# Kernel optimization log

Hardware: AMD Instinct MI355X
Metric: run time of the kernel (lower is better)

## Reference

```python
import jax, jax.numpy as jnp
import numpy as np

N_SH, N_U, N_I = 1195, 805, 390   # hard-coded in KDHR
D = 64                            # embedding_dim / latent_dim
B = 65536                         # prescription batch
E_SH = 100000
BN_EPS = 1e-5


def setup_inputs() -> dict:
    key = jax.random.key(0)
    ks = jax.random.split(key, 20)
    s = 0.02
    return {
        "edge_index_SH": jax.random.randint(ks[0], (2, E_SH), 0, N_SH),
        "edge_index_SS": jax.random.randint(ks[1], (2, 50000), 0, N_U),
        "edge_index_HH": jax.random.randint(ks[2], (2, 50000), 0, N_I),
        "prescription": jax.random.uniform(ks[3], (B, N_I), dtype=jnp.float32),
        "sh_emb": jax.random.normal(ks[4], (N_SH, D), dtype=jnp.float32) * s,
        # GCNConv_SH layer 1 and 2 (Linear weights, torch layout [out,in])
        "W1": jax.random.normal(ks[5], (D, D), dtype=jnp.float32) * s,
        "b1": jnp.zeros((D,), jnp.float32),
        "W2": jax.random.normal(ks[6], (D, D), dtype=jnp.float32) * s,
        "b2": jnp.zeros((D,), jnp.float32),
        # proj = Linear(64,64) -> ELU -> Linear(64,64)
        "Wp1": jax.random.normal(ks[7], (D, D), dtype=jnp.float32) * s,
        "bp1": jnp.zeros((D,), jnp.float32),
        "Wp2": jax.random.normal(ks[8], (D, D), dtype=jnp.float32) * s,
        "bp2": jnp.zeros((D,), jnp.float32),
        # self.mlp = Linear(64,64); self.SI_bn = BatchNorm1d(64)
        "Wm": jax.random.normal(ks[9], (D, D), dtype=jnp.float32) * s,
        "bm": jnp.zeros((D,), jnp.float32),
        "bn_gamma": jnp.ones((D,), jnp.float32),
        "bn_beta": jnp.zeros((D,), jnp.float32),
    }


def _gcn_layer(x, W, b, src, dst):
    # GCNConv_SH: message = lin(x_j), aggr='mean' at dst, then tanh
    m = x[src] @ W.T + b                                   # [E, D]
    s = jax.ops.segment_sum(m, dst, num_segments=N_SH)     # [N_SH, D]
    cnt = jax.ops.segment_sum(jnp.ones(dst.shape, x.dtype), dst, num_segments=N_SH)
    return jnp.tanh(s / jnp.maximum(cnt, 1.0)[:, None])


def _l2n(z):
    return z / jnp.linalg.norm(z, axis=1, keepdims=True)


def reference(edge_index_SH, edge_index_SS, edge_index_HH, prescription,
              sh_emb, W1, b1, W2, b2, Wp1, bp1, Wp2, bp2, Wm, bm,
              bn_gamma, bn_beta):
    src, dst = edge_index_SH[0], edge_index_SH[1]
    h1 = _gcn_layer(sh_emb, W1, b1, src, dst)
    h2 = _gcn_layer(h1, W2, b2, src, dst)                  # x_SH6
    c_emb_u, c_emb_i = h2[:N_U], h2[N_U:]                  # [805,64], [390,64]

    def proj(z):
        return jax.nn.elu(z @ Wp1.T + bp1) @ Wp2.T + bp2

    # Same2Loss projected+normalized embeddings (c_u: herbs 390, c_i: users 805)
    es = _l2n(proj(c_emb_i))                               # [390, 64]
    eh = _l2n(proj(c_emb_u))                               # [805, 64]

    e_synd = prescription @ es                             # [B, 64]
    pre_sum = jnp.sum(prescription, axis=1, keepdims=True)
    e = e_synd / pre_sum
    e = e @ Wm.T + bm                                      # mlp
    mu = jnp.mean(e, axis=0)                               # BatchNorm1d (train)
    var = jnp.var(e, axis=0)
    e = (e - mu) * jax.lax.rsqrt(var + BN_EPS) * bn_gamma + bn_beta
    e = jax.nn.relu(e)
    return e @ eh.T                                        # [B, 805]
```

## Files before the change

kernel.cpp:

```cpp
#include <hip/hip_runtime.h>
#include <math.h>

#define NSH 1195
#define NU  805
#define NI  390
#define DD  64
#define BROWS 65536
#define ESH 100000
#define KPAD 416
#define NUPAD 832

typedef _Float16 f16;
typedef _Float16 f16x2 __attribute__((ext_vector_type(2)));
typedef _Float16 f16x8 __attribute__((ext_vector_type(8)));
typedef float f32x4 __attribute__((ext_vector_type(4)));

#define OFF_STATS  0u
#define OFF_ESWT   128u
#define OFF_EH     13440u
#define OFF_ROWPTR 41344u
#define OFF_CURSOR 42624u
#define OFF_COLIDX 43904u
#define OFF_H1     144000u
#define OFF_EPRE   220480u

__global__ __launch_bounds__(1024) void prep_kernel(const int* __restrict__ edges,
                                                    int* __restrict__ row_ptr,
                                                    int* __restrict__ cursor,
                                                    float* __restrict__ stats,
                                                    f16* __restrict__ esWT) {
    __shared__ int s[2048];
    __shared__ int h[1280];
    int t = threadIdx.x;
    h[t] = 0;
    if (t + 1024 < 1280) h[t + 1024] = 0;
    if (t < 128) stats[t] = 0.f;
    if (t < 832) {
        int d = t / 13, j = t - d * 13;
        *(uint32_t*)&esWT[d * KPAD + 390 + j * 2] = 0u;
    }
    __syncthreads();
    for (int e = t; e < ESH; e += 1024)
        atomicAdd(&h[edges[ESH + e]], 1);
    __syncthreads();
    s[t] = (t < NSH) ? h[t] : 0;
    s[t + 1024] = (t + 1024 < NSH) ? h[t + 1024] : 0;
    __syncthreads();
    for (int off = 1; off < 2048; off <<= 1) {
        int a = s[t], b = s[t + 1024];
        int aa = (t >= off) ? s[t - off] : 0;
        int bb = s[t + 1024 - off];
        __syncthreads();
        s[t] = a + aa;
        s[t + 1024] = b + bb;
        __syncthreads();
    }
    if (t == 0) row_ptr[0] = 0;
    for (int i = t; i < NSH; i += 1024) {
        row_ptr[i + 1] = s[i];
        cursor[i] = (i == 0) ? 0 : s[i - 1];
    }
}

__global__ __launch_bounds__(256) void scatter_kernel(const int* __restrict__ edges,
                                                      int* __restrict__ cursor,
                                                      int* __restrict__ col_idx) {
    int e = blockIdx.x * 256 + threadIdx.x;
    if (e < ESH) {
        int t = edges[ESH + e];
        int pos = atomicAdd(&cursor[t], 1);
        col_idx[pos] = edges[e];
    }
}

__global__ __launch_bounds__(256) void gcn_gather1(const int* __restrict__ row_ptr,
                                                   const int* __restrict__ col_idx,
                                                   const float* __restrict__ x,
                                                   const float* __restrict__ W,
                                                   const float* __restrict__ b,
                                                   float* __restrict__ out) {
    __shared__ float s_wt[DD * DD];
    __shared__ float s_p[4 * DD];
    int tid = threadIdx.x;
    int w = tid >> 6, lane = tid & 63;
    for (int i = tid; i < DD * DD; i += 256) {
        int j = i >> 6, k = i & 63;
        s_wt[k * DD + j] = W[i];
    }
    int node = blockIdx.x;
    int beg = row_ptr[node], end = row_ptr[node + 1];
    float acc = 0.f;
    for (int e = beg + w; e < end; e += 4)
        acc += x[col_idx[e] * DD + lane];
    s_p[w * DD + lane] = acc;
    __syncthreads();
    float z = s_p[lane] + s_p[DD + lane] + s_p[2 * DD + lane] + s_p[3 * DD + lane];
    __syncthreads();
    if (w == 0) s_p[lane] = z;
    __syncthreads();
    float cntf = (float)(end - beg);
    float o = cntf * b[lane];
    #pragma unroll 8
    for (int k = 0; k < DD; k++)
        o = fmaf(s_p[k], s_wt[k * DD + lane], o);
    float h = tanhf(o / fmaxf(cntf, 1.f));
    if (w == 0) out[node * DD + lane] = h;
}

__global__ __launch_bounds__(256) void gcn2_fused(const int* __restrict__ row_ptr,
                                                  const int* __restrict__ col_idx,
                                                  const float* __restrict__ h1,
                                                  const float* __restrict__ W2,
                                                  const float* __restrict__ b2,
                                                  const float* __restrict__ Wp1,
                                                  const float* __restrict__ bp1,
                                                  const float* __restrict__ Wp2,
                                                  const float* __restrict__ bp2,
                                                  const float* __restrict__ Wm,
                                                  f16* __restrict__ eh16,
                                                  f16* __restrict__ esWT) {
    __shared__ float s_w2[DD * DD], s_p1[DD * DD], s_p2[DD * DD], s_wm[DD * DD];
    __shared__ float s_v[4 * DD];
    int tid = threadIdx.x;
    int w = tid >> 6, lane = tid & 63;
    for (int i = tid; i < DD * DD; i += 256) {
        int j = i >> 6, k = i & 63;
        s_w2[k * DD + j] = W2[i];
        s_p1[k * DD + j] = Wp1[i];
        s_p2[k * DD + j] = Wp2[i];
        s_wm[k * DD + j] = Wm[i];
    }
    int node = blockIdx.x;
    int beg = row_ptr[node], end = row_ptr[node + 1];
    float acc = 0.f;
    for (int e = beg + w; e < end; e += 4)
        acc += h1[col_idx[e] * DD + lane];
    s_v[w * DD + lane] = acc;
    __syncthreads();
    float z = s_v[lane] + s_v[DD + lane] + s_v[2 * DD + lane] + s_v[3 * DD + lane];
    __syncthreads();
    if (w == 0) s_v[lane] = z;
    __syncthreads();
    float cntf = (float)(end - beg);
    float o = cntf * b2[lane];
    #pragma unroll 8
    for (int k = 0; k < DD; k++)
        o = fmaf(s_v[k], s_w2[k * DD + lane], o);
    float h2v = tanhf(o / fmaxf(cntf, 1.f));
    __syncthreads();
    if (w == 0) s_v[lane] = h2v;
    __syncthreads();
    float t = bp1[lane];
    #pragma unroll 8
    for (int k = 0; k < DD; k++)
        t = fmaf(s_v[k], s_p1[k * DD + lane], t);
    t = t > 0.f ? t : expm1f(t);
    __syncthreads();
    if (w == 0) s_v[lane] = t;
    __syncthreads();
    float o2 = bp2[lane];
    #pragma unroll 8
    for (int k = 0; k < DD; k++)
        o2 = fmaf(s_v[k], s_p2[k * DD + lane], o2);
    float sq = o2 * o2;
    #pragma unroll
    for (int off = 1; off < 64; off <<= 1) sq += __shfl_xor(sq, off);
    float r = o2 / sqrtf(sq);
    if (node < NU) {
        if (w == 0) eh16[node * DD + lane] = (f16)r;
    } else {
        __syncthreads();
        if (w == 0) s_v[lane] = r;
        __syncthreads();
        float m = 0.f;
        #pragma unroll 8
        for (int k = 0; k < DD; k++)
            m = fmaf(s_v[k], s_wm[k * DD + lane], m);
        if (w == 0) esWT[lane * KPAD + (node - NU)] = (f16)m;
    }
}

__global__ __launch_bounds__(256) void synd_v2(const float* __restrict__ P,
                                               const f16* __restrict__ esWT,
                                               const float* __restrict__ bm,
                                               float* __restrict__ e_pre,
                                               float* __restrict__ stats) {
    __shared__ __align__(16) f16 s_P[64 * KPAD];
    __shared__ float s_stats[128];
    int tid = threadIdx.x;
    if (tid < 128) s_stats[tid] = 0.f;

    for (int i = tid; i < 64 * 13; i += 256) {
        int row = i / 13, j = i - row * 13;
        *(uint32_t*)&s_P[row * KPAD + 390 + j * 2] = 0u;
    }
    const float* Pb = P + (size_t)blockIdx.x * 64 * NI;
    for (int it = 0; it < 25; it++) {
        int f = it * 1024 + tid * 4;
        if (f < 64 * NI) {
            f32x4 v = *(const f32x4*)(Pb + f);
            int row = f / NI;
            int col = f - row * NI;
            *(f16x2*)&s_P[row * KPAD + col] = (f16x2){(f16)v.x, (f16)v.y};
            int row2 = row, col2 = col + 2;
            if (col2 == NI) { row2 = row + 1; col2 = 0; }
            *(f16x2*)&s_P[row2 * KPAD + col2] = (f16x2){(f16)v.z, (f16)v.w};
        }
    }
    __syncthreads();

    int lane = tid & 63, w = tid >> 6;
    int l15 = lane & 15, lk = lane >> 4;
    int rowbase = blockIdx.x * 64 + w * 16;

    f32x4 acc[5];
    #pragma unroll
    for (int ni = 0; ni < 5; ni++) acc[ni] = (f32x4){0.f, 0.f, 0.f, 0.f};

    f16x8 ones;
    #pragma unroll
    for (int i = 0; i < 8; i++) ones[i] = (f16)1.0f;

    const f16* arow = &s_P[(w * 16 + l15) * KPAD];
    const f16* bp[4];
    #pragma unroll
    for (int ni = 0; ni < 4; ni++)
        bp[ni] = esWT + (size_t)(ni * 16 + l15) * KPAD;

    for (int step = 0; step < 13; step++) {
        int kb = step * 32 + lk * 8;
        f16x8 a = *(const f16x8*)(arow + kb);
        f16x8 bfr[4];
        #pragma unroll
        for (int ni = 0; ni < 4; ni++)
            bfr[ni] = *(const f16x8*)(bp[ni] + kb);
        #pragma unroll
        for (int ni = 0; ni < 4; ni++)
            acc[ni] = __builtin_amdgcn_mfma_f32_16x16x32_f16(a, bfr[ni], acc[ni], 0, 0, 0);
        acc[4] = __builtin_amdgcn_mfma_f32_16x16x32_f16(a, ones, acc[4], 0, 0, 0);
    }

    float bmv[4];
    #pragma unroll
    for (int ni = 0; ni < 4; ni++) bmv[ni] = bm[ni * 16 + l15];

    #pragma unroll
    for (int ni = 0; ni < 4; ni++) {
        float s = 0.f, q = 0.f;
        #pragma unroll
        for (int j = 0; j < 4; j++) {
            float v = acc[ni][j] / acc[4][j] + bmv[ni];
            int row = rowbase + lk * 4 + j;
            e_pre[(size_t)row * DD + ni * 16 + l15] = v;
            s += v;
            q = fmaf(v, v, q);
        }
        s += __shfl_xor(s, 16); s += __shfl_xor(s, 32);
        q += __shfl_xor(q, 16); q += __shfl_xor(q, 32);
        if (lk == 0) {
            atomicAdd(&s_stats[ni * 16 + l15], s);
            atomicAdd(&s_stats[64 + ni * 16 + l15], q);
        }
    }
    __syncthreads();
    if (tid < 128) atomicAdd(&stats[tid], s_stats[tid]);
}

__global__ __launch_bounds__(256) void out_fused(const float* __restrict__ e_pre,
                                                 const f16* __restrict__ eh16,
                                                 const float* __restrict__ stats,
                                                 const float* __restrict__ gamma,
                                                 const float* __restrict__ beta,
                                                 float* __restrict__ out) {
    __shared__ __align__(16) f16 s_eh[256 * DD];
    __shared__ float s_bn[128];
    int tid = threadIdx.x;
    int cg = blockIdx.x;
    int t0 = (cg == 0) ? 0 : cg * 3 + 1;
    int nt = (cg == 0) ? 4 : 3;
    int cbase = t0 * 64;
    int nrows = nt * 64;

    if (tid < 64) {
        float mu  = stats[tid] * (1.0f / 65536.0f);
        float ex2 = stats[64 + tid] * (1.0f / 65536.0f);
        float var = ex2 - mu * mu;
        float rstd = 1.0f / sqrtf(var + 1e-5f);
        float sc = rstd * gamma[tid];
        s_bn[tid] = sc;
        s_bn[64 + tid] = beta[tid] - mu * sc;
    }

    const uint4* src = (const uint4*)(eh16 + (size_t)cbase * DD);
    int nchunks = nrows * 8;
    for (int c = tid; c < nchunks; c += 256) {
        int row = c >> 3, slot = c & 7;
        uint4 v = src[c];
        *(uint4*)&s_eh[row * DD + ((slot ^ (row & 7)) << 3)] = v;
    }
    __syncthreads();

    int lane = tid & 63, w = tid >> 6;
    int l15 = lane & 15, lk = lane >> 4;
    int r0 = blockIdx.y * 64 + w * 16;

    f16x8 afr[2];
    {
        const float* pr = e_pre + (size_t)(r0 + l15) * DD;
        #pragma unroll
        for (int ks = 0; ks < 2; ks++) {
            int kb = ks * 32 + lk * 8;
            f32x4 v0 = *(const f32x4*)&pr[kb];
            f32x4 v1 = *(const f32x4*)&pr[kb + 4];
            f16x8 a;
            #pragma unroll
            for (int i = 0; i < 4; i++) {
                a[i]     = (f16)fmaxf(fmaf(v0[i], s_bn[kb + i],     s_bn[64 + kb + i]),     0.f);
                a[4 + i] = (f16)fmaxf(fmaf(v1[i], s_bn[kb + 4 + i], s_bn[64 + kb + 4 + i]), 0.f);
            }
            afr[ks] = a;
        }
    }

    for (int tt = 0; tt < nt; tt++) {
        f32x4 acc[4];
        #pragma unroll
        for (int c16 = 0; c16 < 4; c16++) acc[c16] = (f32x4){0.f, 0.f, 0.f, 0.f};
        #pragma unroll
        for (int c16 = 0; c16 < 4; c16++) {
            int lc = tt * 64 + c16 * 16 + l15;
            #pragma unroll
            for (int ks = 0; ks < 2; ks++) {
                int slot = (ks * 4 + lk) ^ (lc & 7);
                f16x8 b = *(const f16x8*)&s_eh[lc * DD + (slot << 3)];
                acc[c16] = __builtin_amdgcn_mfma_f32_16x16x32_f16(afr[ks], b, acc[c16], 0, 0, 0);
            }
        }
        #pragma unroll
        for (int c16 = 0; c16 < 4; c16++) {
            int col = cbase + tt * 64 + c16 * 16 + l15;
            if (col < NU) {
                #pragma unroll
                for (int j = 0; j < 4; j++) {
                    int row = r0 + lk * 4 + j;
                    out[(size_t)row * NU + col] = acc[c16][j];
                }
            }
        }
    }
}

extern "C" void kernel_launch(void* const* d_in, const int* in_sizes, int n_in,
                              void* d_out, int out_size, void* d_ws, size_t ws_size,
                              hipStream_t stream) {
    const int*   eSH   = (const int*)d_in[0];
    const float* presc = (const float*)d_in[3];
    const float* shemb = (const float*)d_in[4];
    const float* W1  = (const float*)d_in[5];
    const float* b1  = (const float*)d_in[6];
    const float* W2  = (const float*)d_in[7];
    const float* b2  = (const float*)d_in[8];
    const float* Wp1 = (const float*)d_in[9];
    const float* bp1 = (const float*)d_in[10];
    const float* Wp2 = (const float*)d_in[11];
    const float* bp2 = (const float*)d_in[12];
    const float* Wm  = (const float*)d_in[13];
    const float* bm  = (const float*)d_in[14];
    const float* gam = (const float*)d_in[15];
    const float* bet = (const float*)d_in[16];

    float* ws    = (float*)d_ws;
    float* stats = ws + OFF_STATS;
    f16*   esWT  = (f16*)(ws + OFF_ESWT);
    f16*   eh16  = (f16*)(ws + OFF_EH);
    int*   rowp  = (int*)(ws + OFF_ROWPTR);
    int*   curs  = (int*)(ws + OFF_CURSOR);
    int*   cidx  = (int*)(ws + OFF_COLIDX);
    float* h1    = ws + OFF_H1;
    float* e_pre = ws + OFF_EPRE;
    float* out   = (float*)d_out;

    prep_kernel<<<1, 1024, 0, stream>>>(eSH, rowp, curs, stats, esWT);
    scatter_kernel<<<391, 256, 0, stream>>>(eSH, curs, cidx);
    gcn_gather1<<<NSH, 256, 0, stream>>>(rowp, cidx, shemb, W1, b1, h1);
    gcn2_fused<<<NSH, 256, 0, stream>>>(rowp, cidx, h1, W2, b2,
                                        Wp1, bp1, Wp2, bp2, Wm, eh16, esWT);
    synd_v2<<<1024, 256, 0, stream>>>(presc, esWT, bm, e_pre, stats);
    out_fused<<<dim3(4, 1024), 256, 0, stream>>>(e_pre, eh16, stats, gam, bet, out);
}
```

Measured before the change: 241.9 us.

## Replace CSR graph aggregation with dense adjacency matrix MFMA GEMMs

Drops the CSR build (single-block histogram/scan plus scatter) and per-node gather kernels. Instead it builds a dense fp32 count adjacency matrix with atomics and runs both GCN layers plus the projection MLPs as fp16 MFMA matrix multiplies over 64-node tiles. Degree counts come from an extra MFMA against a ones vector. This removes the serial prep kernel and irregular gathers, but adds zeroing and reading of a ~1216x1216 dense matrix, runs the graph stage on only 19 blocks, and lowers the graph stage to fp16 precision. The matrix reuses the e_pre workspace, which is safe only because it is consumed before synd_v2 writes e_pre.

```diff
diff --git a/kernel.cpp b/kernel.cpp
--- a/kernel.cpp
+++ b/kernel.cpp
@@ -9,6 +9,7 @@
 #define ESH 100000
 #define KPAD 416
 #define NUPAD 832
+#define KA  1216
 
 typedef _Float16 f16;
 typedef _Float16 f16x2 __attribute__((ext_vector_type(2)));
@@ -18,166 +19,240 @@
 #define OFF_STATS  0u
 #define OFF_ESWT   128u
 #define OFF_EH     13440u
-#define OFF_ROWPTR 41344u
-#define OFF_CURSOR 42624u
-#define OFF_COLIDX 43904u
-#define OFF_H1     144000u
-#define OFF_EPRE   220480u
-
-__global__ __launch_bounds__(1024) void prep_kernel(const int* __restrict__ edges,
-                                                    int* __restrict__ row_ptr,
-                                                    int* __restrict__ cursor,
-                                                    float* __restrict__ stats,
-                                                    f16* __restrict__ esWT) {
-    __shared__ int s[2048];
-    __shared__ int h[1280];
-    int t = threadIdx.x;
-    h[t] = 0;
-    if (t + 1024 < 1280) h[t + 1024] = 0;
-    if (t < 128) stats[t] = 0.f;
-    if (t < 832) {
-        int d = t / 13, j = t - d * 13;
-        *(uint32_t*)&esWT[d * KPAD + 390 + j * 2] = 0u;
-    }
+#define OFF_SHEMBT 40064u
+#define OFF_H1T    78976u
+#define OFF_EPRE   117888u
+
+__global__ __launch_bounds__(256) void prep_kernel(const float* __restrict__ shemb,
+                                                   float* __restrict__ A,
+                                                   f16* __restrict__ shembT,
+                                                   float* __restrict__ stats,
+                                                   f16* __restrict__ esWT,
+                                                   f16* __restrict__ eh16) {
+    int b = blockIdx.x, tid = threadIdx.x;
+    if (b < 1444) {
+        int i = b * 256 + tid;
+        *(f32x4*)&A[i * 4] = (f32x4){0.f, 0.f, 0.f, 0.f};
+    } else if (b < 1748) {
+        int i = (b - 1444) * 256 + tid;
+        int d = i / KA, k = i - d * KA;
+        shembT[i] = (k < NSH) ? (f16)shemb[k * DD + d] : (f16)0.f;
+    } else {
+        for (int i = tid; i < 128; i += 256) stats[i] = 0.f;
+        for (int i = tid; i < 832; i += 256) {
+            int d = i / 13, j = i - d * 13;
+            *(uint32_t*)&esWT[d * KPAD + 390 + j * 2] = 0u;
+        }
+        for (int i = tid; i < 864; i += 256)
+            ((uint32_t*)eh16)[NU * 32 + i] = 0u;
+    }
+}
+
+__global__ __launch_bounds__(256) void build_A(const int* __restrict__ edges,
+                                               float* __restrict__ A) {
+    int e = blockIdx.x * 256 + threadIdx.x;
+    if (e < ESH)
+        atomicAdd(&A[edges[ESH + e] * KA + edges[e]], 1.0f);
+}
+
+__global__ __launch_bounds__(256) void gcn1_mfma(const float* __restrict__ A,
+                                                 const f16* __restrict__ shembT,
+                                                 const float* __restrict__ W1,
+                                                 const float* __restrict__ b1,
+                                                 f16* __restrict__ h1T) {
+    __shared__ __align__(16) f16 s_w1[DD * 72];
+    __shared__ __align__(16) f16 s_agg[4][16 * 72];
+    int tid = threadIdx.x;
+    for (int i = tid; i < DD * DD; i += 256)
+        s_w1[(i >> 6) * 72 + (i & 63)] = (f16)W1[i];
     __syncthreads();
-    for (int e = t; e < ESH; e += 1024)
-        atomicAdd(&h[edges[ESH + e]], 1);
+
+    int lane = tid & 63, w = tid >> 6;
+    int l15 = lane & 15, lk = lane >> 4;
+    int mbase = blockIdx.x * 64 + w * 16;
+
+    f16x8 ones;
+    #pragma unroll
+    for (int i = 0; i < 8; i++) ones[i] = (f16)1.0f;
+
+    f32x4 acc[4], accC = (f32x4){0.f, 0.f, 0.f, 0.f};
+    #pragma unroll
+    for (int ni = 0; ni < 4; ni++) acc[ni] = (f32x4){0.f, 0.f, 0.f, 0.f};
+    const float* arow = A + (size_t)(mbase + l15) * KA;
+    for (int step = 0; step < 38; step++) {
+        int kb = step * 32 + lk * 8;
+        f32x4 q0 = *(const f32x4*)(arow + kb);
+        f32x4 q1 = *(const f32x4*)(arow + kb + 4);
+        f16x8 a;
+        a[0] = (f16)q0.x; a[1] = (f16)q0.y; a[2] = (f16)q0.z; a[3] = (f16)q0.w;
+        a[4] = (f16)q1.x; a[5] = (f16)q1.y; a[6] = (f16)q1.z; a[7] = (f16)q1.w;
+        #pragma unroll
+        for (int ni = 0; ni < 4; ni++) {
+            f16x8 bf = *(const f16x8*)&shembT[(ni * 16 + l15) * KA + kb];
+            acc[ni] = __builtin_amdgcn_mfma_f32_16x16x32_f16(a, bf, acc[ni], 0, 0, 0);
+        }
+        accC = __builtin_amdgcn_mfma_f32_16x16x32_f16(a, ones, accC, 0, 0, 0);
+    }
+    #pragma unroll
+    for (int ni = 0; ni < 4; ni++)
+        #pragma unroll
+        for (int j = 0; j < 4; j++)
+            s_agg[w][(lk * 4 + j) * 72 + ni * 16 + l15] = (f16)acc[ni][j];
+
+    f16x8 a2[2];
+    a2[0] = *(const f16x8*)&s_agg[w][l15 * 72 + lk * 8];
+    a2[1] = *(const f16x8*)&s_agg[w][l15 * 72 + 32 + lk * 8];
+    f32x4 p[4];
+    #pragma unroll
+    for (int ni = 0; ni < 4; ni++) p[ni] = (f32x4){0.f, 0.f, 0.f, 0.f};
+    #pragma unroll
+    for (int ks = 0; ks < 2; ks++)
+        #pragma unroll
+        for (int ni = 0; ni < 4; ni++) {
+            f16x8 bf = *(const f16x8*)&s_w1[(ni * 16 + l15) * 72 + ks * 32 + lk * 8];
+            p[ni] = __builtin_amdgcn_mfma_f32_16x16x32_f16(a2[ks], bf, p[ni], 0, 0, 0);
+        }
+    #pragma unroll
+    for (int ni = 0; ni < 4; ni++) {
+        int n = ni * 16 + l15;
+        float bn = b1[n];
+        #pragma unroll
+        for (int j = 0; j < 4; j++) {
+            float cnt = accC[j];
+            float h = tanhf(fmaf(cnt, bn, p[ni][j]) / fmaxf(cnt, 1.f));
+            h1T[n * KA + mbase + lk * 4 + j] = (f16)h;
+        }
+    }
+}
+
+__global__ __launch_bounds__(256) void gcn2_mfma(const float* __restrict__ A,
+                                                 const f16* __restrict__ h1T,
+                                                 const float* __restrict__ W2,
+                                                 const float* __restrict__ b2,
+                                                 const float* __restrict__ Wp1,
+                                                 const float* __restrict__ bp1,
+                                                 const float* __restrict__ Wp2,
+                                                 const float* __restrict__ bp2,
+                                                 const float* __restrict__ Wm,
+                                                 f16* __restrict__ eh16,
+                                                 f16* __restrict__ esWT) {
+    __shared__ __align__(16) f16 s_w2[DD * 72], s_p1[DD * 72], s_p2[DD * 72], s_wm[DD * 72];
+    __shared__ __align__(16) f16 s_buf[4][16 * 72];
+    __shared__ __align__(16) float s_o2[4][16 * 68];
+    int tid = threadIdx.x;
+    for (int i = tid; i < DD * DD; i += 256) {
+        int n = i >> 6, k = i & 63;
+        s_w2[n * 72 + k] = (f16)W2[i];
+        s_p1[n * 72 + k] = (f16)Wp1[i];
+        s_p2[n * 72 + k] = (f16)Wp2[i];
+        s_wm[n * 72 + k] = (f16)Wm[i];
+    }
     __syncthreads();
-    s[t] = (t < NSH) ? h[t] : 0;
-    s[t + 1024] = (t + 1024 < NSH) ? h[t + 1024] : 0;
-    __syncthreads();
-    for (int off = 1; off < 2048; off <<= 1) {
-        int a = s[t], b = s[t + 1024];
-        int aa = (t >= off) ? s[t - off] : 0;
-        int bb = s[t + 1024 - off];
-        __syncthreads();
-        s[t] = a + aa;
-        s[t + 1024] = b + bb;
-        __syncthreads();
-    }
-    if (t == 0) row_ptr[0] = 0;
-    for (int i = t; i < NSH; i += 1024) {
-        row_ptr[i + 1] = s[i];
-        cursor[i] = (i == 0) ? 0 : s[i - 1];
-    }
-}
-
-__global__ __launch_bounds__(256) void scatter_kernel(const int* __restrict__ edges,
-                                                      int* __restrict__ cursor,
-                                                      int* __restrict__ col_idx) {
-    int e = blockIdx.x * 256 + threadIdx.x;
-    if (e < ESH) {
-        int t = edges[ESH + e];
-        int pos = atomicAdd(&cursor[t], 1);
-        col_idx[pos] = edges[e];
-    }
-}
-
-__global__ __launch_bounds__(256) void gcn_gather1(const int* __restrict__ row_ptr,
-                                                   const int* __restrict__ col_idx,
-                                                   const float* __restrict__ x,
-                                                   const float* __restrict__ W,
-                                                   const float* __restrict__ b,
-                                                   float* __restrict__ out) {
-    __shared__ float s_wt[DD * DD];
-    __shared__ float s_p[4 * DD];
-    int tid = threadIdx.x;
-    int w = tid >> 6, lane = tid & 63;
-    for (int i = tid; i < DD * DD; i += 256) {
-        int j = i >> 6, k = i & 63;
-        s_wt[k * DD + j] = W[i];
-    }
-    int node = blockIdx.x;
-    int beg = row_ptr[node], end = row_ptr[node + 1];
-    float acc = 0.f;
-    for (int e = beg + w; e < end; e += 4)
-        acc += x[col_idx[e] * DD + lane];
-    s_p[w * DD + lane] = acc;
-    __syncthreads();
-    float z = s_p[lane] + s_p[DD + lane] + s_p[2 * DD + lane] + s_p[3 * DD + lane];
-    __syncthreads();
-    if (w == 0) s_p[lane] = z;
-    __syncthreads();
-    float cntf = (float)(end - beg);
-    float o = cntf * b[lane];
-    #pragma unroll 8
-    for (int k = 0; k < DD; k++)
-        o = fmaf(s_p[k], s_wt[k * DD + lane], o);
-    float h = tanhf(o / fmaxf(cntf, 1.f));
-    if (w == 0) out[node * DD + lane] = h;
-}
-
-__global__ __launch_bounds__(256) void gcn2_fused(const int* __restrict__ row_ptr,
-                                                  const int* __restrict__ col_idx,
-                                                  const float* __restrict__ h1,
-                                                  const float* __restrict__ W2,
-                                                  const float* __restrict__ b2,
-                                                  const float* __restrict__ Wp1,
-                                                  const float* __restrict__ bp1,
-                                                  const float* __restrict__ Wp2,
-                                                  const float* __restrict__ bp2,
-                                                  const float* __restrict__ Wm,
-                                                  f16* __restrict__ eh16,
-                                                  f16* __restrict__ esWT) {
-    __shared__ float s_w2[DD * DD], s_p1[DD * DD], s_p2[DD * DD], s_wm[DD * DD];
-    __shared__ float s_v[4 * DD];
-    int tid = threadIdx.x;
-    int w = tid >> 6, lane = tid & 63;
-    for (int i = tid; i < DD * DD; i += 256) {
-        int j = i >> 6, k = i & 63;
-        s_w2[k * DD + j] = W2[i];
-        s_p1[k * DD + j] = Wp1[i];
-        s_p2[k * DD + j] = Wp2[i];
-        s_wm[k * DD + j] = Wm[i];
-    }
-    int node = blockIdx.x;
-    int beg = row_ptr[node], end = row_ptr[node + 1];
-    float acc = 0.f;
-    for (int e = beg + w; e < end; e += 4)
-        acc += h1[col_idx[e] * DD + lane];
-    s_v[w * DD + lane] = acc;
-    __syncthreads();
-    float z = s_v[lane] + s_v[DD + lane] + s_v[2 * DD + lane] + s_v[3 * DD + lane];
-    __syncthreads();
-    if (w == 0) s_v[lane] = z;
-    __syncthreads();
-    float cntf = (float)(end - beg);
-    float o = cntf * b2[lane];
-    #pragma unroll 8
-    for (int k = 0; k < DD; k++)
-        o = fmaf(s_v[k], s_w2[k * DD + lane], o);
-    float h2v = tanhf(o / fmaxf(cntf, 1.f));
-    __syncthreads();
-    if (w == 0) s_v[lane] = h2v;
-    __syncthreads();
-    float t = bp1[lane];
-    #pragma unroll 8
-    for (int k = 0; k < DD; k++)
-        t = fmaf(s_v[k], s_p1[k * DD + lane], t);
-    t = t > 0.f ? t : expm1f(t);
-    __syncthreads();
-    if (w == 0) s_v[lane] = t;
-    __syncthreads();
-    float o2 = bp2[lane];
-    #pragma unroll 8
-    for (int k = 0; k < DD; k++)
-        o2 = fmaf(s_v[k], s_p2[k * DD + lane], o2);
-    float sq = o2 * o2;
-    #pragma unroll
-    for (int off = 1; off < 64; off <<= 1) sq += __shfl_xor(sq, off);
-    float r = o2 / sqrtf(sq);
-    if (node < NU) {
-        if (w == 0) eh16[node * DD + lane] = (f16)r;
-    } else {
-        __syncthreads();
-        if (w == 0) s_v[lane] = r;
-        __syncthreads();
-        float m = 0.f;
-        #pragma unroll 8
-        for (int k = 0; k < DD; k++)
-            m = fmaf(s_v[k], s_wm[k * DD + lane], m);
-        if (w == 0) esWT[lane * KPAD + (node - NU)] = (f16)m;
-    }
+
+    int lane = tid & 63, w = tid >> 6;
+    int l15 = lane & 15, lk = lane >> 4;
+    int mbase = blockIdx.x * 64 + w * 16;
+
+    f16x8 ones;
+    #pragma unroll
+    for (int i = 0; i < 8; i++) ones[i] = (f16)1.0f;
+
+    f32x4 acc[4], accC = (f32x4){0.f, 0.f, 0.f, 0.f};
+    #pragma unroll
+    for (int ni = 0; ni < 4; ni++) acc[ni] = (f32x4){0.f, 0.f, 0.f, 0.f};
+    const float* arow = A + (size_t)(mbase + l15) * KA;
+    for (int step = 0; step < 38; step++) {
+        int kb = step * 32 + lk * 8;
+        f32x4 q0 = *(const f32x4*)(arow + kb);
+        f32x4 q1 = *(const f32x4*)(arow + kb + 4);
+        f16x8 a;
+        a[0] = (f16)q0.x; a[1] = (f16)q0.y; a[2] = (f16)q0.z; a[3] = (f16)q0.w;
+        a[4] = (f16)q1.x; a[5] = (f16)q1.y; a[6] = (f16)q1.z; a[7] = (f16)q1.w;
+        #pragma unroll
+        for (int ni = 0; ni < 4; ni++) {
+            f16x8 bf = *(const f16x8*)&h1T[(ni * 16 + l15) * KA + kb];
+            acc[ni] = __builtin_amdgcn_mfma_f32_16x16x32_f16(a, bf, acc[ni], 0, 0, 0);
+        }
+        accC = __builtin_amdgcn_mfma_f32_16x16x32_f16(a, ones, accC, 0, 0, 0);
+    }
+    #pragma unroll
+    for (int ni = 0; ni < 4; ni++)
+        #pragma unroll
+        for (int j = 0; j < 4; j++)
+            s_buf[w][(lk * 4 + j) * 72 + ni * 16 + l15] = (f16)acc[ni][j];
+
+    #define GEMM64(SWT, POUT)                                                        \
+    {                                                                                \
+        f16x8 a2[2];                                                                 \
+        a2[0] = *(const f16x8*)&s_buf[w][l15 * 72 + lk * 8];                         \
+        a2[1] = *(const f16x8*)&s_buf[w][l15 * 72 + 32 + lk * 8];                    \
+        _Pragma("unroll")                                                            \
+        for (int ni = 0; ni < 4; ni++) POUT[ni] = (f32x4){0.f, 0.f, 0.f, 0.f};       \
+        _Pragma("unroll")                                                            \
+        for (int ks = 0; ks < 2; ks++)                                               \
+            _Pragma("unroll")                                                        \
+            for (int ni = 0; ni < 4; ni++) {                                         \
+                f16x8 bf = *(const f16x8*)&SWT[(ni * 16 + l15) * 72 + ks * 32 + lk * 8]; \
+                POUT[ni] = __builtin_amdgcn_mfma_f32_16x16x32_f16(a2[ks], bf, POUT[ni], 0, 0, 0); \
+            }                                                                        \
+    }
+
+    f32x4 p[4];
+    GEMM64(s_w2, p);
+    #pragma unroll
+    for (int ni = 0; ni < 4; ni++) {
+        int n = ni * 16 + l15;
+        float bn = b2[n];
+        #pragma unroll
+        for (int j = 0; j < 4; j++) {
+            float cnt = accC[j];
+            float h = tanhf(fmaf(cnt, bn, p[ni][j]) / fmaxf(cnt, 1.f));
+            s_buf[w][(lk * 4 + j) * 72 + n] = (f16)h;
+        }
+    }
+    GEMM64(s_p1, p);
+    #pragma unroll
+    for (int ni = 0; ni < 4; ni++) {
+        int n = ni * 16 + l15;
+        float bn = bp1[n];
+        #pragma unroll
+        for (int j = 0; j < 4; j++) {
+            float t = p[ni][j] + bn;
+            t = t > 0.f ? t : expm1f(t);
+            s_buf[w][(lk * 4 + j) * 72 + n] = (f16)t;
+        }
+    }
+    GEMM64(s_p2, p);
+    #pragma unroll
+    for (int ni = 0; ni < 4; ni++) {
+        int n = ni * 16 + l15;
+        float bn = bp2[n];
+        #pragma unroll
+        for (int j = 0; j < 4; j++)
+            s_o2[w][(lk * 4 + j) * 68 + n] = p[ni][j] + bn;
+    }
+    for (int r = 0; r < 16; r++) {
+        float v = s_o2[w][r * 68 + lane];
+        float sq = v * v;
+        #pragma unroll
+        for (int off = 1; off < 64; off <<= 1) sq += __shfl_xor(sq, off);
+        float rr = v / sqrtf(sq);
+        int node = mbase + r;
+        if (node < NU) eh16[node * DD + lane] = (f16)rr;
+        s_buf[w][r * 72 + lane] = (f16)rr;
+    }
+    GEMM64(s_wm, p);
+    #pragma unroll
+    for (int ni = 0; ni < 4; ni++) {
+        int n = ni * 16 + l15;
+        #pragma unroll
+        for (int j = 0; j < 4; j++) {
+            int node = mbase + lk * 4 + j;
+            if (node >= NU && node < NSH)
+                esWT[n * KPAD + (node - NU)] = (f16)p[ni][j];
+        }
+    }
+    #undef GEMM64
 }
 
 __global__ __launch_bounds__(256) void synd_v2(const float* __restrict__ P,
@@ -369,22 +444,20 @@
     const float* gam = (const float*)d_in[15];
     const float* bet = (const float*)d_in[16];
 
-    float* ws    = (float*)d_ws;
-    float* stats = ws + OFF_STATS;
-    f16*   esWT  = (f16*)(ws + OFF_ESWT);
-    f16*   eh16  = (f16*)(ws + OFF_EH);
-    int*   rowp  = (int*)(ws + OFF_ROWPTR);
-    int*   curs  = (int*)(ws + OFF_CURSOR);
-    int*   cidx  = (int*)(ws + OFF_COLIDX);
-    float* h1    = ws + OFF_H1;
-    float* e_pre = ws + OFF_EPRE;
-    float* out   = (float*)d_out;
-
-    prep_kernel<<<1, 1024, 0, stream>>>(eSH, rowp, curs, stats, esWT);
-    scatter_kernel<<<391, 256, 0, stream>>>(eSH, curs, cidx);
-    gcn_gather1<<<NSH, 256, 0, stream>>>(rowp, cidx, shemb, W1, b1, h1);
-    gcn2_fused<<<NSH, 256, 0, stream>>>(rowp, cidx, h1, W2, b2,
-                                        Wp1, bp1, Wp2, bp2, Wm, eh16, esWT);
+    float* ws     = (float*)d_ws;
+    float* stats  = ws + OFF_STATS;
+    f16*   esWT   = (f16*)(ws + OFF_ESWT);
+    f16*   eh16   = (f16*)(ws + OFF_EH);
+    f16*   shembT = (f16*)(ws + OFF_SHEMBT);
+    f16*   h1T    = (f16*)(ws + OFF_H1T);
+    float* e_pre  = ws + OFF_EPRE;
+    float* A      = ws + OFF_EPRE;
+    float* out    = (float*)d_out;
+
+    prep_kernel<<<1749, 256, 0, stream>>>(shemb, A, shembT, stats, esWT, eh16);
+    build_A<<<391, 256, 0, stream>>>(eSH, A);
+    gcn1_mfma<<<19, 256, 0, stream>>>(A, shembT, W1, b1, h1T);
+    gcn2_mfma<<<19, 256, 0, stream>>>(A, h1T, W2, b2, Wp1, bp1, Wp2, bp2, Wm, eh16, esWT);
     synd_v2<<<1024, 256, 0, stream>>>(presc, esWT, bm, e_pre, stats);
     out_fused<<<dim3(4, 1024), 256, 0, stream>>>(e_pre, eh16, stats, gam, bet, out);
 }
```

After: 221.4 us. 8.5% less time.
